# Performance work log

Hardware: AMD Instinct MI355X
Metric: run time of the kernel (lower is better)

Reference implementation:

```python
import jax, jax.numpy as jnp
import numpy as np

B, I, H = 4096, 1024, 1024


def setup_inputs() -> dict:
    key = jax.random.key(0)
    ks = jax.random.split(key, 7)
    s = 0.1  # matches uniform(-0.1, 0.1) init scale loosely
    return {
        "input": jax.random.normal(ks[0], (B, I), jnp.float32),
        "h_t": jax.random.normal(ks[1], (B, H), jnp.float32),
        "c_t": jax.random.normal(ks[2], (B, H), jnp.float32),
        "w_i": jax.random.uniform(ks[3], (I, 4 * H), jnp.float32, -s, s),
        "w_h": jax.random.uniform(ks[4], (H, 4 * H), jnp.float32, -s, s),
        "b_i": jax.random.uniform(ks[5], (4 * H,), jnp.float32, -s, s),
        "b_h": jax.random.uniform(ks[6], (4 * H,), jnp.float32, -s, s),
    }


def reference(input, h_t, c_t, w_i, w_h, b_i, b_h):
    # ifgo: [B, 4H] = x @ w_i + h @ w_h + b_i + b_h
    ifgo = input @ w_i + h_t @ w_h + (b_i + b_h)
    i, f, g, o = jnp.split(ifgo, 4, axis=1)
    i = jax.nn.sigmoid(i)
    f = jax.nn.sigmoid(f)
    g = jnp.tanh(g)
    o = jax.nn.sigmoid(o)
    c_new = f * c_t + i * g
    h_new = o * jnp.tanh(c_new)
    return (h_new, c_new)
```

## Files before the change

kernel.cpp:

```cpp
#include <hip/hip_runtime.h>
#include <stdint.h>

typedef __attribute__((ext_vector_type(8))) short short8;
typedef __attribute__((ext_vector_type(4))) float floatx4;

__device__ inline unsigned short f2bf(float x) {
  union { float f; unsigned int u; } v; v.f = x;
  unsigned int r = v.u + 0x7FFFu + ((v.u >> 16) & 1u);
  return (unsigned short)(r >> 16);
}

__global__ void pack_all(const float* __restrict__ x, const float* __restrict__ h,
                         const float* __restrict__ wi, const float* __restrict__ wh,
                         unsigned short* __restrict__ A,
                         unsigned short* __restrict__ Wt) {
  int bid = blockIdx.x;
  int t = threadIdx.x;
  if (bid < 4096) {
    int idx = bid * 256 + t;
    int row = idx >> 8;
    int kc  = (idx & 255) << 3;
    const float* src = (kc < 1024) ? (x + (size_t)row * 1024 + kc)
                                   : (h + (size_t)row * 1024 + (kc - 1024));
    float4 a = ((const float4*)src)[0];
    float4 b = ((const float4*)src)[1];
    uint4 o;
    o.x = f2bf(a.x) | ((unsigned)f2bf(a.y) << 16);
    o.y = f2bf(a.z) | ((unsigned)f2bf(a.w) << 16);
    o.z = f2bf(b.x) | ((unsigned)f2bf(b.y) << 16);
    o.w = f2bf(b.z) | ((unsigned)f2bf(b.w) << 16);
    *(uint4*)(A + (size_t)row * 2048 + kc) = o;
  } else {
    __shared__ float tile[64][65];
    int b2 = bid - 4096;
    int kt = b2 & 31;
    int nt = b2 >> 5;
    int k0 = kt << 6, n0 = nt << 6;
    const float* src = (k0 < 1024) ? (wi + (size_t)k0 * 4096)
                                   : (wh + (size_t)(k0 - 1024) * 4096);
    int c4 = (t & 15) << 2, rr = t >> 4;
#pragma unroll
    for (int p = 0; p < 4; ++p) {
      int kk = rr + p * 16;
      float4 v = *(const float4*)(src + (size_t)kk * 4096 + n0 + c4);
      tile[kk][c4 + 0] = v.x; tile[kk][c4 + 1] = v.y;
      tile[kk][c4 + 2] = v.z; tile[kk][c4 + 3] = v.w;
    }
    __syncthreads();
    int k8 = (t & 7) << 3, nn = t >> 3;
#pragma unroll
    for (int p = 0; p < 2; ++p) {
      int n = n0 + nn + p * 32;
      int hh = n & 1023, g = n >> 10;
      int R = ((hh >> 5) << 7) + (((hh >> 4) & 1) << 6) + (g << 4) + (hh & 15);
      int nl = nn + p * 32;
      uint4 o;
      o.x = f2bf(tile[k8 + 0][nl]) | ((unsigned)f2bf(tile[k8 + 1][nl]) << 16);
      o.y = f2bf(tile[k8 + 2][nl]) | ((unsigned)f2bf(tile[k8 + 3][nl]) << 16);
      o.z = f2bf(tile[k8 + 4][nl]) | ((unsigned)f2bf(tile[k8 + 5][nl]) << 16);
      o.w = f2bf(tile[k8 + 6][nl]) | ((unsigned)f2bf(tile[k8 + 7][nl]) << 16);
      *(uint4*)(Wt + (size_t)R * 2048 + k0 + k8) = o;
    }
  }
}

__device__ inline void gl_lds16(const void* g, void* l) {
  __builtin_amdgcn_global_load_lds(
      (const __attribute__((address_space(1))) void*)g,
      (__attribute__((address_space(3))) void*)l, 16, 0, 0);
}

__device__ inline float sigm(float x)  { return 1.0f / (1.0f + __expf(-x)); }
__device__ inline float tanhx(float x) { return 2.0f / (1.0f + __expf(-2.0f * x)) - 1.0f; }

#define MFMA_BF16 __builtin_amdgcn_mfma_f32_16x16x32_bf16

#define STAGE2(SRC, DSTARR, DOFF)                                    \
  do {                                                               \
    gl_lds16((SRC) + rOff, (DSTARR) + (DOFF) + tid * 16);            \
    gl_lds16((SRC) + rOff + (size_t)64 * 4096,                       \
             (DSTARR) + (DOFF) + tid * 16 + 8192);                   \
  } while (0)

#define MFMA16(I0)                                                            \
  _Pragma("unroll")                                                           \
  for (int j = 0; j < 4; ++j) {                                               \
    acc[(I0)][j]     = MFMA_BF16(a0k0, bf[j][0], acc[(I0)][j], 0, 0, 0);      \
    acc[(I0) + 1][j] = MFMA_BF16(a1k0, bf[j][0], acc[(I0) + 1][j], 0, 0, 0);  \
  }                                                                           \
  _Pragma("unroll")                                                           \
  for (int j = 0; j < 4; ++j) {                                               \
    acc[(I0)][j]     = MFMA_BF16(a0k1, bf[j][1], acc[(I0)][j], 0, 0, 0);      \
    acc[(I0) + 1][j] = MFMA_BF16(a1k1, bf[j][1], acc[(I0) + 1][j], 0, 0, 0);  \
  }

#define PHASE(CA, I0, STAGE_STMT, TAIL_STMT)                                  \
  {                                                                           \
    const char* pa_ = (const char*)(CA) + aRowOff;                            \
    short8 a0k0 = *(const short8*)(pa_ + (I0) * 2048 + c0);                   \
    short8 a1k0 = *(const short8*)(pa_ + ((I0) + 1) * 2048 + c0);             \
    short8 a0k1 = *(const short8*)(pa_ + (I0) * 2048 + c1);                   \
    short8 a1k1 = *(const short8*)(pa_ + ((I0) + 1) * 2048 + c1);             \
    STAGE_STMT;                                                               \
    __builtin_amdgcn_s_barrier();                                             \
    __builtin_amdgcn_s_setprio(1);                                            \
    MFMA16(I0)                                                                \
    __builtin_amdgcn_s_setprio(0);                                            \
    TAIL_STMT;                                                                \
    __builtin_amdgcn_s_barrier();                                             \
  }

#define PHASE0(CA, CB, STAGE_STMT)                                            \
  {                                                                           \
    const char* pb_ = (const char*)(CB) + bRowOff;                            \
    const char* pa_ = (const char*)(CA) + aRowOff;                            \
    _Pragma("unroll")                                                         \
    for (int j = 0; j < 4; ++j) {                                             \
      bf[j][0] = *(const short8*)(pb_ + j * 2048 + c0);                       \
      bf[j][1] = *(const short8*)(pb_ + j * 2048 + c1);                       \
    }                                                                         \
    short8 a0k0 = *(const short8*)(pa_ + c0);                                 \
    short8 a1k0 = *(const short8*)(pa_ + 2048 + c0);                          \
    short8 a0k1 = *(const short8*)(pa_ + c1);                                 \
    short8 a1k1 = *(const short8*)(pa_ + 2048 + c1);                          \
    STAGE_STMT;                                                               \
    __builtin_amdgcn_s_barrier();                                             \
    __builtin_amdgcn_s_setprio(1);                                            \
    MFMA16(0)                                                                 \
    __builtin_amdgcn_s_setprio(0);                                            \
    __builtin_amdgcn_s_barrier();                                             \
  }

#define TILE(CA, CB, NA, AN, BN)                                              \
  {                                                                           \
    const char* aS = aBase + (size_t)(((AN) & 31) << 7);                      \
    const char* bS = bBase + (size_t)(((BN) & 31) << 7);                      \
    short8 bf[4][2];                                                          \
    PHASE0(CA, CB, STAGE2(aS, NA, 0));                                        \
    PHASE(CA, 2, STAGE2(aS + (size_t)128 * 4096, NA, 16384), );               \
    PHASE(CA, 4, STAGE2(bS, CB, 0), );                                        \
    PHASE(CA, 6, STAGE2(bS + (size_t)128 * 4096, CB, 16384),                  \
          asm volatile("s_waitcnt vmcnt(4)" ::: "memory"));                   \
  }

__global__ void __launch_bounds__(512, 2) gemm_lstm(
    const unsigned short* __restrict__ A,
    const unsigned short* __restrict__ Bt,
    const float* __restrict__ ct,
    const float* __restrict__ bi,
    const float* __restrict__ bh,
    float* __restrict__ out) {
  __shared__ __align__(16) char A0[32768];
  __shared__ __align__(16) char A1[32768];
  __shared__ __align__(16) char B0[32768];
  __shared__ __align__(16) char B1[32768];

  const int tid  = threadIdx.x;
  const int lane = tid & 63;
  const int wave = tid >> 6;
  const int wm = wave >> 2;
  const int wn = wave & 3;

  const int bid = blockIdx.x;
  const int gx = bid & 7;
  const int sx = bid >> 3;
  const int bx = (gx << 1) + (sx & 1);
  const int by = sx >> 1;
  const int m0 = by << 8;

  const int ec = lane & 15;
  const int h  = (bx << 6) + ((wn >> 1) << 5) + ((wn & 1) << 4) + ec;
  float bias[4];
#pragma unroll
  for (int j = 0; j < 4; ++j) bias[j] = bi[j * 1024 + h] + bh[j * 1024 + h];

  const int sr = tid >> 3;
  const unsigned swz = (unsigned)(((tid & 7) ^ (sr & 7)) << 4);
  const size_t rOff = (size_t)sr * 4096 + swz;
  const char* aBase = (const char*)A  + (size_t)m0 * 4096;
  const char* bBase = (const char*)Bt + (size_t)(bx << 8) * 4096;

  const int lr  = lane & 15;
  const int kq  = lane >> 4;
  const int key = lane & 7;
  const int c0  = (kq ^ key) << 4;
  const int c1  = ((4 + kq) ^ key) << 4;
  const int aRowOff = ((wm << 7) + lr) * 128;
  const int bRowOff = ((wn << 6) + lr) * 128;

  floatx4 acc[8][4] = {};

  STAGE2(bBase, B0, 0);
  STAGE2(bBase + (size_t)128 * 4096, B0, 16384);
  STAGE2(aBase, A0, 0);
  STAGE2(aBase + (size_t)128 * 4096, A0, 16384);
  STAGE2(bBase + 128, B1, 0);
  STAGE2(bBase + 128 + (size_t)128 * 4096, B1, 16384);
  asm volatile("s_waitcnt vmcnt(4)" ::: "memory");
  __builtin_amdgcn_s_barrier();

  for (int it = 0; it < 16; ++it) {
    const int t = it << 1;
    TILE(A0, B0, A1, t + 1, t + 2);
    TILE(A1, B1, A0, t + 2, t + 3);
  }

  const int er = (lane >> 4) << 2;
  float cv[8][4];
#pragma unroll
  for (int i = 0; i < 8; ++i)
#pragma unroll
    for (int rg = 0; rg < 4; ++rg) {
      int row = m0 + (wm << 7) + i * 16 + er + rg;
      cv[i][rg] = ct[(size_t)row * 1024 + h];
    }
#pragma unroll
  for (int i = 0; i < 8; ++i) {
#pragma unroll
    for (int rg = 0; rg < 4; ++rg) {
      int row = m0 + (wm << 7) + i * 16 + er + rg;
      size_t o = (size_t)row * 1024 + h;
      float iv = sigm(acc[i][0][rg] + bias[0]);
      float fv = sigm(acc[i][1][rg] + bias[1]);
      float gv = tanhx(acc[i][2][rg] + bias[2]);
      float ov = sigm(acc[i][3][rg] + bias[3]);
      float cn = fv * cv[i][rg] + iv * gv;
      out[o] = ov * tanhx(cn);
      out[4194304 + o] = cn;
    }
  }
}

extern "C" void kernel_launch(void* const* d_in, const int* in_sizes, int n_in,
                              void* d_out, int out_size, void* d_ws, size_t ws_size,
                              hipStream_t stream) {
  const float* x  = (const float*)d_in[0];
  const float* ht = (const float*)d_in[1];
  const float* ct = (const float*)d_in[2];
  const float* wi = (const float*)d_in[3];
  const float* wh = (const float*)d_in[4];
  const float* bi = (const float*)d_in[5];
  const float* bh = (const float*)d_in[6];
  float* out = (float*)d_out;

  char* ws = (char*)d_ws;
  unsigned short* Abf = (unsigned short*)ws;
  unsigned short* Wbf = (unsigned short*)(ws + (16u << 20));

  pack_all<<<6144, 256, 0, stream>>>(x, ht, wi, wh, Abf, Wbf);
  gemm_lstm<<<256, 512, 0, stream>>>(Abf, Wbf, ct, bi, bh, out);
}
```

Baseline: 199.3 us.

## Restructure GEMM main loop into software-pipelined LDS fragment prefetch phases

Rewrites the per-tile inner loop so each phase issues LDS reads for the next phase's A/B fragments before running the current 16 MFMAs, using explicit lgkmcnt waits. The first fragments of the next tile are prefetched at the end of the current tile and carried across in register arrays. The goal is to hide LDS read latency behind MFMA work and drop one barrier per phase. In exchange it uses more VGPRs, which could spill or cut occupancy, and the hand-tuned waitcnt values risk races or stalls.

```diff
diff --git a/kernel.cpp b/kernel.cpp
--- a/kernel.cpp
+++ b/kernel.cpp
@@ -82,65 +82,74 @@
              (DSTARR) + (DOFF) + tid * 16 + 8192);                   \
   } while (0)
 
-#define MFMA16(I0)                                                            \
-  _Pragma("unroll")                                                           \
-  for (int j = 0; j < 4; ++j) {                                               \
-    acc[(I0)][j]     = MFMA_BF16(a0k0, bf[j][0], acc[(I0)][j], 0, 0, 0);      \
-    acc[(I0) + 1][j] = MFMA_BF16(a1k0, bf[j][0], acc[(I0) + 1][j], 0, 0, 0);  \
-  }                                                                           \
-  _Pragma("unroll")                                                           \
-  for (int j = 0; j < 4; ++j) {                                               \
-    acc[(I0)][j]     = MFMA_BF16(a0k1, bf[j][1], acc[(I0)][j], 0, 0, 0);      \
-    acc[(I0) + 1][j] = MFMA_BF16(a1k1, bf[j][1], acc[(I0) + 1][j], 0, 0, 0);  \
-  }
-
-#define PHASE(CA, I0, STAGE_STMT, TAIL_STMT)                                  \
-  {                                                                           \
-    const char* pa_ = (const char*)(CA) + aRowOff;                            \
-    short8 a0k0 = *(const short8*)(pa_ + (I0) * 2048 + c0);                   \
-    short8 a1k0 = *(const short8*)(pa_ + ((I0) + 1) * 2048 + c0);             \
-    short8 a0k1 = *(const short8*)(pa_ + (I0) * 2048 + c1);                   \
-    short8 a1k1 = *(const short8*)(pa_ + ((I0) + 1) * 2048 + c1);             \
-    STAGE_STMT;                                                               \
-    __builtin_amdgcn_s_barrier();                                             \
-    __builtin_amdgcn_s_setprio(1);                                            \
-    MFMA16(I0)                                                                \
-    __builtin_amdgcn_s_setprio(0);                                            \
-    TAIL_STMT;                                                                \
-    __builtin_amdgcn_s_barrier();                                             \
-  }
-
-#define PHASE0(CA, CB, STAGE_STMT)                                            \
-  {                                                                           \
-    const char* pb_ = (const char*)(CB) + bRowOff;                            \
-    const char* pa_ = (const char*)(CA) + aRowOff;                            \
-    _Pragma("unroll")                                                         \
-    for (int j = 0; j < 4; ++j) {                                             \
-      bf[j][0] = *(const short8*)(pb_ + j * 2048 + c0);                       \
-      bf[j][1] = *(const short8*)(pb_ + j * 2048 + c1);                       \
-    }                                                                         \
-    short8 a0k0 = *(const short8*)(pa_ + c0);                                 \
-    short8 a1k0 = *(const short8*)(pa_ + 2048 + c0);                          \
-    short8 a0k1 = *(const short8*)(pa_ + c1);                                 \
-    short8 a1k1 = *(const short8*)(pa_ + 2048 + c1);                          \
-    STAGE_STMT;                                                               \
-    __builtin_amdgcn_s_barrier();                                             \
-    __builtin_amdgcn_s_setprio(1);                                            \
-    MFMA16(0)                                                                 \
-    __builtin_amdgcn_s_setprio(0);                                            \
-    __builtin_amdgcn_s_barrier();                                             \
-  }
-
-#define TILE(CA, CB, NA, AN, BN)                                              \
+#define TILE(CA, CB, NA, NB, PBIN, PAIN, PBOUT, PAOUT, AN, BN)                \
   {                                                                           \
     const char* aS = aBase + (size_t)(((AN) & 31) << 7);                      \
     const char* bS = bBase + (size_t)(((BN) & 31) << 7);                      \
-    short8 bf[4][2];                                                          \
-    PHASE0(CA, CB, STAGE2(aS, NA, 0));                                        \
-    PHASE(CA, 2, STAGE2(aS + (size_t)128 * 4096, NA, 16384), );               \
-    PHASE(CA, 4, STAGE2(bS, CB, 0), );                                        \
-    PHASE(CA, 6, STAGE2(bS + (size_t)128 * 4096, CB, 16384),                  \
-          asm volatile("s_waitcnt vmcnt(4)" ::: "memory"));                   \
+    const char* pa_ = (const char*)(CA) + aRowOff;                            \
+    const char* pb_ = (const char*)(CB) + bRowOff;                            \
+    short8 bk1[4], a1f[4], a2f[4], a3f[4];                                    \
+                 \
+    __builtin_amdgcn_s_barrier();                                             \
+    _Pragma("unroll")                                                         \
+    for (int j = 0; j < 4; ++j) bk1[j] = *(const short8*)(pb_ + j * 2048 + c1); \
+    _Pragma("unroll")                                                         \
+    for (int i = 0; i < 4; ++i) a1f[i] = *(const short8*)(pa_ + i * 2048 + c1); \
+    STAGE2(aS, NA, 0);                                                        \
+    asm volatile("s_waitcnt lgkmcnt(8)" ::: "memory");                        \
+    __builtin_amdgcn_s_setprio(1);                                            \
+    _Pragma("unroll")                                                         \
+    for (int i = 0; i < 4; ++i)                                               \
+      _Pragma("unroll")                                                       \
+      for (int j = 0; j < 4; ++j)                                             \
+        acc[i][j] = MFMA_BF16(PAIN[i], PBIN[j], acc[i][j], 0, 0, 0);          \
+    __builtin_amdgcn_s_setprio(0);                                            \
+                               \
+    __builtin_amdgcn_s_barrier();                                             \
+    _Pragma("unroll")                                                         \
+    for (int i = 0; i < 4; ++i) a2f[i] = *(const short8*)(pa_ + (4 + i) * 2048 + c0); \
+    STAGE2(aS + (size_t)128 * 4096, NA, 16384);                               \
+    asm volatile("s_waitcnt lgkmcnt(4)" ::: "memory");                        \
+    __builtin_amdgcn_s_setprio(1);                                            \
+    _Pragma("unroll")                                                         \
+    for (int i = 0; i < 4; ++i)                                               \
+      _Pragma("unroll")                                                       \
+      for (int j = 0; j < 4; ++j)                                             \
+        acc[i][j] = MFMA_BF16(a1f[i], bk1[j], acc[i][j], 0, 0, 0);            \
+    __builtin_amdgcn_s_setprio(0);                                            \
+                \
+    __builtin_amdgcn_s_barrier();                                             \
+    _Pragma("unroll")                                                         \
+    for (int i = 0; i < 4; ++i) a3f[i] = *(const short8*)(pa_ + (4 + i) * 2048 + c1); \
+    STAGE2(bS, CB, 0);                                                        \
+    asm volatile("s_waitcnt lgkmcnt(4)" ::: "memory");                        \
+    __builtin_amdgcn_s_setprio(1);                                            \
+    _Pragma("unroll")                                                         \
+    for (int i = 0; i < 4; ++i)                                               \
+      _Pragma("unroll")                                                       \
+      for (int j = 0; j < 4; ++j)                                             \
+        acc[4 + i][j] = MFMA_BF16(a2f[i], PBIN[j], acc[4 + i][j], 0, 0, 0);   \
+    __builtin_amdgcn_s_setprio(0);                                            \
+    asm volatile("s_waitcnt vmcnt(2)" ::: "memory");                          \
+                \
+    __builtin_amdgcn_s_barrier();                                             \
+    {                                                                         \
+      const char* na_ = (const char*)(NA) + aRowOff;                          \
+      const char* nb_ = (const char*)(NB) + bRowOff;                          \
+      _Pragma("unroll")                                                       \
+      for (int j = 0; j < 4; ++j) PBOUT[j] = *(const short8*)(nb_ + j * 2048 + c0); \
+      _Pragma("unroll")                                                       \
+      for (int i = 0; i < 4; ++i) PAOUT[i] = *(const short8*)(na_ + i * 2048 + c0); \
+    }                                                                         \
+    STAGE2(bS + (size_t)128 * 4096, CB, 16384);                               \
+    asm volatile("s_waitcnt lgkmcnt(8)" ::: "memory");                        \
+    __builtin_amdgcn_s_setprio(1);                                            \
+    _Pragma("unroll")                                                         \
+    for (int i = 0; i < 4; ++i)                                               \
+      _Pragma("unroll")                                                       \
+      for (int j = 0; j < 4; ++j)                                             \
+        acc[4 + i][j] = MFMA_BF16(a3f[i], bk1[j], acc[4 + i][j], 0, 0, 0);    \
+    __builtin_amdgcn_s_setprio(0);                                            \
   }
 
 __global__ void __launch_bounds__(512, 2) gemm_lstm(
@@ -189,6 +198,7 @@
   const int bRowOff = ((wn << 6) + lr) * 128;
 
   floatx4 acc[8][4] = {};
+  short8 pb0[4], pa0[4], pb1[4], pa1[4];
 
   STAGE2(bBase, B0, 0);
   STAGE2(bBase + (size_t)128 * 4096, B0, 16384);
@@ -198,11 +208,19 @@
   STAGE2(bBase + 128 + (size_t)128 * 4096, B1, 16384);
   asm volatile("s_waitcnt vmcnt(4)" ::: "memory");
   __builtin_amdgcn_s_barrier();
+  {
+    const char* pbp = (const char*)B0 + bRowOff;
+    const char* pap = (const char*)A0 + aRowOff;
+#pragma unroll
+    for (int j = 0; j < 4; ++j) pb0[j] = *(const short8*)(pbp + j * 2048 + c0);
+#pragma unroll
+    for (int i = 0; i < 4; ++i) pa0[i] = *(const short8*)(pap + i * 2048 + c0);
+  }
 
   for (int it = 0; it < 16; ++it) {
     const int t = it << 1;
-    TILE(A0, B0, A1, t + 1, t + 2);
-    TILE(A1, B1, A0, t + 2, t + 3);
+    TILE(A0, B0, A1, B1, pb0, pa0, pb1, pa1, t + 1, t + 2);
+    TILE(A1, B1, A0, B0, pb1, pa1, pb0, pa0, t + 2, t + 3);
   }
 
   const int er = (lane >> 4) << 2;
```

Measured after the change: 195.2 us. 2.1% less time.
